# Kernel optimization log

Measured on AMD Instinct MI355X. Metric: run time of the kernel, lower is better.

Reference implementation:

```python
import jax, jax.numpy as jnp
import numpy as np

N_NODES = 50000
N_EDGES = 800000
D = 64
N_GRAPHS = 500  # 100 nodes per graph


def setup_inputs() -> dict:
    key = jax.random.key(0)
    k1, k2, k3, k4, k5, k6 = jax.random.split(key, 6)
    x = jax.random.normal(k1, (N_NODES, D), dtype=jnp.float32)
    edge_index = jax.random.randint(k2, (2, N_EDGES), 0, N_NODES, dtype=jnp.int32)
    split_n = jnp.full((N_GRAPHS,), N_NODES // N_GRAPHS, dtype=jnp.int32)
    # edge_att_mlp: Linear(2*D, 1)
    W_edge = jax.random.normal(k3, (2 * D, 1), dtype=jnp.float32) * 0.05
    b_edge = jax.random.normal(k4, (1,), dtype=jnp.float32) * 0.05
    # node_att_cov: GCNConv(D, 1)
    W_gcn = jax.random.normal(k5, (D, 1), dtype=jnp.float32) * 0.05
    b_gcn = jax.random.normal(k6, (1,), dtype=jnp.float32) * 0.05
    return {"x": x, "edge_index": edge_index, "split_n": split_n,
            "W_edge": W_edge, "b_edge": b_edge, "W_gcn": W_gcn, "b_gcn": b_gcn}


def _segment_softmax(v, seg, num_segments):
    # softmax over dim 0 within each segment (replaces lazy_soft's python loop)
    m = jax.ops.segment_max(v, seg, num_segments=num_segments)
    e = jnp.exp(v - m[seg])
    s = jax.ops.segment_sum(e, seg, num_segments=num_segments)
    return e / s[seg]


def reference(x, edge_index, split_n, W_edge, b_edge, W_gcn, b_gcn):
    n = x.shape[0]
    row, col = edge_index[0], edge_index[1]

    # edge attention: gather pair, linear, sigmoid
    edge_rep = jnp.concatenate([x[row], x[col]], axis=-1)  # [E, 2D]
    edge_att = jax.nn.sigmoid(edge_rep @ W_edge + b_edge)  # [E, 1]
    edge_att_m = edge_att
    edge_att_s = 1.0 - edge_att

    # GCNConv(D, 1): add self-loops, symmetric deg^-1/2 norm, linear, scatter-sum
    h = x @ W_gcn  # [N, 1]
    loop = jnp.arange(n, dtype=row.dtype)
    src = jnp.concatenate([row, loop])
    dst = jnp.concatenate([col, loop])
    deg = jnp.zeros((n,), dtype=x.dtype).at[dst].add(1.0)
    dinv = jax.lax.rsqrt(deg)  # deg >= 1 due to self-loops
    norm = dinv[src] * dinv[dst]  # [E+N]
    node_att = jax.ops.segment_sum(norm[:, None] * h[src], dst, num_segments=n) + b_gcn

    # per-graph ragged softmax (fused segment softmax)
    seg = jnp.repeat(jnp.arange(split_n.shape[0]), split_n, total_repeat_length=n)
    node_att_m = _segment_softmax(node_att, seg, split_n.shape[0])
    node_att_s = _segment_softmax(1.0 - node_att_m, seg, split_n.shape[0])
    return edge_att_m, edge_att_s, node_att_m, node_att_s
```

## Files before the change

### kernel.cpp

```cpp
#include <hip/hip_runtime.h>
#include <math.h>


#define RANGE_S 16384
#define RANGE_H 32768
#define BD_H 1024
#define SOFT_LDS_CAP 2048

typedef unsigned short u16t;
typedef unsigned int u32t;

__global__ __launch_bounds__(BD_H)
void k1_node_hist(const float* __restrict__ x,
                  const float* __restrict__ W_edge,
                  const float* __restrict__ W_gcn,
                  const int* __restrict__ ei,
                  float* __restrict__ pa, float* __restrict__ pb,
                  float* __restrict__ hbuf,
                  u16t* __restrict__ pd,
                  int N, int E, int Ch, int Rh, int CHh, int nodeBlocks, int vec) {
    __shared__ u32t t32[RANGE_H / 2];
    const int bid = blockIdx.x, tid = threadIdx.x;
    if (bid < nodeBlocks) {
        float4* Wsh = (float4*)t32;
        if (tid < 32) Wsh[tid] = ((const float4*)W_edge)[tid];
        else if (tid < 48) Wsh[tid] = ((const float4*)W_gcn)[tid - 32];
        __syncthreads();
        int lane = tid & 15;
        long long gid = (long long)bid * BD_H + tid;
        int i = (int)(gid >> 4);
        if (i >= N) return;
        float4 v = ((const float4*)(x + (size_t)i * 64))[lane];
        float4 wa = Wsh[lane], wb = Wsh[16 + lane], wg = Wsh[32 + lane];
        float p1 = v.x*wa.x + v.y*wa.y + v.z*wa.z + v.w*wa.w;
        float p2 = v.x*wb.x + v.y*wb.y + v.z*wb.z + v.w*wb.w;
        float p3 = v.x*wg.x + v.y*wg.y + v.z*wg.z + v.w*wg.w;
#pragma unroll
        for (int s = 1; s < 16; s <<= 1) {
            p1 += __shfl_xor(p1, s);
            p2 += __shfl_xor(p2, s);
            p3 += __shfl_xor(p3, s);
        }
        if (lane == 0) {
            pa[i] = p1;
            pb[i] = p2;
            hbuf[i] = p3;
        }
        return;
    }
    const int hb = bid - nodeBlocks;
    const int c = hb / Rh;
    const int r = hb - c * Rh;
    const int lo = r * RANGE_H;
    for (int j = tid; j < RANGE_H / 2; j += BD_H) t32[j] = 0u;
    __syncthreads();
    const int e_lo = c * CHh;
    const int e_hi = (E < e_lo + CHh) ? E : (e_lo + CHh);
    const int* __restrict__ col = ei + E;
    for (int e = e_lo + tid * 4; e < e_hi; e += BD_H * 4) {
        if (vec && e + 3 < e_hi) {
            int4 cc = *(const int4*)(col + e);
            unsigned u;
            u = (unsigned)(cc.x - lo); if (u < RANGE_H) atomicAdd(&t32[u >> 1], 1u << ((u & 1) << 4));
            u = (unsigned)(cc.y - lo); if (u < RANGE_H) atomicAdd(&t32[u >> 1], 1u << ((u & 1) << 4));
            u = (unsigned)(cc.z - lo); if (u < RANGE_H) atomicAdd(&t32[u >> 1], 1u << ((u & 1) << 4));
            u = (unsigned)(cc.w - lo); if (u < RANGE_H) atomicAdd(&t32[u >> 1], 1u << ((u & 1) << 4));
        } else {
            int ee = (e_hi < e + 4) ? e_hi : e + 4;
            for (int q = e; q < ee; ++q) {
                unsigned u = (unsigned)(col[q] - lo);
                if (u < RANGE_H) atomicAdd(&t32[u >> 1], 1u << ((u & 1) << 4));
            }
        }
    }
    __syncthreads();
    const size_t base = (size_t)c * N;
    for (int j = tid; j < RANGE_H; j += BD_H) {
        int node = lo + j;
        if (node < N)
            pd[base + node] = (u16t)(t32[j >> 1] >> ((j & 1) << 4));
    }
}

__global__ __launch_bounds__(256)
void k2_dinv_sig(const int* __restrict__ ei,
                 const float* __restrict__ pa, const float* __restrict__ pb,
                 const float* __restrict__ b_edge,
                 const u16t* __restrict__ pd,
                 float* __restrict__ hbuf,
                 float* __restrict__ dv1,
                 float* __restrict__ om, float* __restrict__ os,
                 int N, int E, int Ch, int dinvBlocks, int vec) {
    const int bid = blockIdx.x, tid = threadIdx.x;
    if (bid < dinvBlocks) {
        int i = bid * 256 + tid;
        if (i >= N) return;
        unsigned d0 = 1u, d1 = 0u, d2 = 0u, d3 = 0u;
        int c = 0;
        for (; c + 3 < Ch; c += 4) {
            d0 += pd[(size_t)(c + 0) * N + i];
            d1 += pd[(size_t)(c + 1) * N + i];
            d2 += pd[(size_t)(c + 2) * N + i];
            d3 += pd[(size_t)(c + 3) * N + i];
        }
        for (; c < Ch; ++c) d0 += pd[(size_t)c * N + i];
        float dv = rsqrtf((float)((d0 + d1) + (d2 + d3)));
        hbuf[i] *= dv;
        dv1[i] = dv;
        return;
    }
    int t = (bid - dinvBlocks) * 256 + tid;
    int e0 = t * 4;
    const float b = b_edge[0];
    if (vec && e0 + 3 < E) {
        int4 r = *(const int4*)(ei + e0);
        int4 c = *(const int4*)(ei + E + e0);
        float4 m;
        m.x = 1.f / (1.f + expf(-(pa[r.x] + pb[c.x] + b)));
        m.y = 1.f / (1.f + expf(-(pa[r.y] + pb[c.y] + b)));
        m.z = 1.f / (1.f + expf(-(pa[r.z] + pb[c.z] + b)));
        m.w = 1.f / (1.f + expf(-(pa[r.w] + pb[c.w] + b)));
        *(float4*)(om + e0) = m;
        *(float4*)(os + e0) = make_float4(1.f - m.x, 1.f - m.y, 1.f - m.z, 1.f - m.w);
    } else if (e0 < E) {
        int ee = (E < e0 + 4) ? E : e0 + 4;
        for (int e = e0; e < ee; ++e) {
            float a = 1.f / (1.f + expf(-(pa[ei[e]] + pb[ei[E + e]] + b)));
            om[e] = a; os[e] = 1.f - a;
        }
    }
}

__global__ __launch_bounds__(BD_H)
void k3_scat(const int* __restrict__ ei,
             const float* __restrict__ g1,
             float* __restrict__ partial,
             int N, int E, int Cs, int Rs, int CHs, int vec) {
    __shared__ float table[RANGE_S];
    const int tid = threadIdx.x;
    const int c = blockIdx.x / Rs;
    const int r = blockIdx.x - c * Rs;
    const int lo = r * RANGE_S;
    for (int j = tid; j < RANGE_S; j += BD_H) table[j] = 0.f;
    __syncthreads();
    const int e_lo = c * CHs;
    const int e_hi = (E < e_lo + CHs) ? E : (e_lo + CHs);
    const int* __restrict__ row = ei;
    const int* __restrict__ col = ei + E;
    for (int e = e_lo + tid * 4; e < e_hi; e += BD_H * 4) {
        if (vec && e + 3 < e_hi) {
            int4 cc = *(const int4*)(col + e);
            int4 rr = *(const int4*)(row + e);
            unsigned u;
            u = (unsigned)(cc.x - lo); if (u < RANGE_S) atomicAdd(&table[u], g1[rr.x]);
            u = (unsigned)(cc.y - lo); if (u < RANGE_S) atomicAdd(&table[u], g1[rr.y]);
            u = (unsigned)(cc.z - lo); if (u < RANGE_S) atomicAdd(&table[u], g1[rr.z]);
            u = (unsigned)(cc.w - lo); if (u < RANGE_S) atomicAdd(&table[u], g1[rr.w]);
        } else {
            int ee = (e_hi < e + 4) ? e_hi : e + 4;
            for (int q = e; q < ee; ++q) {
                unsigned u = (unsigned)(col[q] - lo);
                if (u < RANGE_S) atomicAdd(&table[u], g1[row[q]]);
            }
        }
    }
    __syncthreads();
    const size_t base = (size_t)c * N;
    for (int j = tid; j < RANGE_S; j += BD_H) {
        int node = lo + j;
        if (node < N) partial[base + node] = table[j];
    }
}

__global__ __launch_bounds__(128)
void k4_softmax(const float* __restrict__ hbuf,
                const float* __restrict__ dv1,
                const float* __restrict__ partial,
                float* __restrict__ accfb,
                const int* __restrict__ split_n,
                float* __restrict__ out_m, float* __restrict__ out_s,
                int N, int Cs) {
    __shared__ float red[128];
    __shared__ int ired[128];
    __shared__ int sh_off;
    __shared__ float sv[SOFT_LDS_CAP];
    const int g = blockIdx.x;
    const int tid = threadIdx.x;
    const int BD = blockDim.x;

    int part = 0;
    for (int j = tid; j < g; j += BD) part += split_n[j];
    ired[tid] = part; __syncthreads();
    for (int s = 64; s > 0; s >>= 1) {
        if (tid < s) ired[tid] += ired[tid + s];
        __syncthreads();
    }
    if (tid == 0) sh_off = ired[0];
    __syncthreads();
    const int off = sh_off;
    const int cnt = split_n[g];
    const bool fits = (cnt <= SOFT_LDS_CAP);

    for (int j = tid; j < cnt; j += BD) {
        int node = off + j;
        float s0 = hbuf[node], s1 = 0.f, s2 = 0.f, s3 = 0.f;
        int c = 0;
        for (; c + 3 < Cs; c += 4) {
            s0 += partial[(size_t)(c + 0) * N + node];
            s1 += partial[(size_t)(c + 1) * N + node];
            s2 += partial[(size_t)(c + 2) * N + node];
            s3 += partial[(size_t)(c + 3) * N + node];
        }
        for (; c < Cs; ++c) s0 += partial[(size_t)c * N + node];
        float a = dv1[node] * ((s0 + s1) + (s2 + s3));
        if (fits) sv[j] = a; else accfb[node] = a;
    }
    __syncthreads();

    float mx = -INFINITY;
    for (int j = tid; j < cnt; j += BD) mx = fmaxf(mx, fits ? sv[j] : accfb[off + j]);
    red[tid] = mx; __syncthreads();
    for (int s = 64; s > 0; s >>= 1) {
        if (tid < s) red[tid] = fmaxf(red[tid], red[tid + s]);
        __syncthreads();
    }
    mx = red[0]; __syncthreads();
    float sum = 0.f;
    for (int j = tid; j < cnt; j += BD) sum += expf((fits ? sv[j] : accfb[off + j]) - mx);
    red[tid] = sum; __syncthreads();
    for (int s = 64; s > 0; s >>= 1) {
        if (tid < s) red[tid] += red[tid + s];
        __syncthreads();
    }
    const float inv1 = 1.0f / red[0]; __syncthreads();
    for (int j = tid; j < cnt; j += BD) {
        float mv = expf((fits ? sv[j] : accfb[off + j]) - mx) * inv1;
        out_m[off + j] = mv;
        if (fits) sv[j] = mv;
    }
    __syncthreads();

    float mx2 = -INFINITY;
    for (int j = tid; j < cnt; j += BD)
        mx2 = fmaxf(mx2, 1.0f - (fits ? sv[j] : out_m[off + j]));
    red[tid] = mx2; __syncthreads();
    for (int s = 64; s > 0; s >>= 1) {
        if (tid < s) red[tid] = fmaxf(red[tid], red[tid + s]);
        __syncthreads();
    }
    mx2 = red[0]; __syncthreads();
    float sum2 = 0.f;
    for (int j = tid; j < cnt; j += BD)
        sum2 += expf(1.0f - (fits ? sv[j] : out_m[off + j]) - mx2);
    red[tid] = sum2; __syncthreads();
    for (int s = 64; s > 0; s >>= 1) {
        if (tid < s) red[tid] += red[tid + s];
        __syncthreads();
    }
    const float inv2 = 1.0f / red[0]; __syncthreads();
    for (int j = tid; j < cnt; j += BD)
        out_s[off + j] = expf(1.0f - (fits ? sv[j] : out_m[off + j]) - mx2) * inv2;
}

extern "C" void kernel_launch(void* const* d_in, const int* in_sizes, int n_in,
                              void* d_out, int out_size, void* d_ws, size_t ws_size,
                              hipStream_t stream) {
    const float* x      = (const float*)d_in[0];
    const int*   ei     = (const int*)d_in[1];
    const int*   splitn = (const int*)d_in[2];
    const float* W_edge = (const float*)d_in[3];
    const float* b_edge = (const float*)d_in[4];
    const float* W_gcn  = (const float*)d_in[5];

    const int N = in_sizes[0] / 64;
    const int E = in_sizes[1] / 2;
    const int G = in_sizes[2];

    float* out = (float*)d_out;
    float* edge_m = out;
    float* edge_s = out + E;
    float* node_m = out + 2LL * E;
    float* node_s = out + 2LL * E + N;

    int Cs = 64;
    while (Cs > 2 && (size_t)(5 + Cs) * N * sizeof(float) > ws_size) Cs >>= 1;
    int Ch = 32;
    while ((E + Ch - 1) / Ch >= 65536) Ch <<= 1;
    const int Rs = (N + RANGE_S - 1) / RANGE_S;
    const int Rh = (N + RANGE_H - 1) / RANGE_H;
    const int CHs = (((E + Cs - 1) / Cs) + 3) & ~3;
    const int CHh = (((E + Ch - 1) / Ch) + 3) & ~3;
    const int vec = ((E & 3) == 0) ? 1 : 0;

    float* pa      = (float*)d_ws;
    float* pb      = pa + N;
    float* hbuf    = pb + N;
    float* dv1     = hbuf + N;
    float* accfb   = dv1 + N;
    float* partial = accfb + N;
    u16t*  pd      = (u16t*)partial;

    const int nodeBlocks = (int)(((long long)N * 16 + BD_H - 1) / BD_H);
    const int dinvBlocks = (N + 255) / 256;
    const int sigBlocks  = ((E + 3) / 4 + 255) / 256;

    k1_node_hist<<<nodeBlocks + Rh * Ch, BD_H, 0, stream>>>(
        x, W_edge, W_gcn, ei, pa, pb, hbuf, pd, N, E, Ch, Rh, CHh, nodeBlocks, vec);
    k2_dinv_sig<<<dinvBlocks + sigBlocks, 256, 0, stream>>>(
        ei, pa, pb, b_edge, pd, hbuf, dv1, edge_m, edge_s, N, E, Ch, dinvBlocks, vec);
    k3_scat<<<Rs * Cs, BD_H, 0, stream>>>(ei, hbuf, partial, N, E, Cs, Rs, CHs, vec);
    k4_softmax<<<G, 128, 0, stream>>>(hbuf, dv1, partial, accfb, splitn,
                                      node_m, node_s, N, Cs);
}
```

Baseline: 52.39 us.

## Move edge sigmoid into scatter kernel and reorder histogram blocks first

The edge-attention sigmoid work now launches as extra blocks of the scatter kernel instead of sharing a launch with the degree/dinv pass. The dinv computation becomes its own small kernel. Histogram blocks are placed before node projection blocks in the first kernel so the long atomic work starts earliest, and the histogram edge-chunk count doubles. The aim is to overlap the bandwidth-bound sigmoid pass with the LDS-atomic scatter and balance block scheduling. The cost is a dinv launch that runs alone, more partial-degree rows for dinv to read, and sigmoid blocks competing for CUs with the scatter.

```diff
diff --git a/kernel.cpp b/kernel.cpp
--- a/kernel.cpp
+++ b/kernel.cpp
@@ -11,23 +11,23 @@
 typedef unsigned int u32t;
 
 __global__ __launch_bounds__(BD_H)
-void k1_node_hist(const float* __restrict__ x,
+void k1_hist_node(const float* __restrict__ x,
                   const float* __restrict__ W_edge,
                   const float* __restrict__ W_gcn,
                   const int* __restrict__ ei,
                   float* __restrict__ pa, float* __restrict__ pb,
                   float* __restrict__ hbuf,
                   u16t* __restrict__ pd,
-                  int N, int E, int Ch, int Rh, int CHh, int nodeBlocks, int vec) {
+                  int N, int E, int Ch, int Rh, int CHh, int histBlocks, int vec) {
     __shared__ u32t t32[RANGE_H / 2];
     const int bid = blockIdx.x, tid = threadIdx.x;
-    if (bid < nodeBlocks) {
+    if (bid >= histBlocks) {
         float4* Wsh = (float4*)t32;
         if (tid < 32) Wsh[tid] = ((const float4*)W_edge)[tid];
         else if (tid < 48) Wsh[tid] = ((const float4*)W_gcn)[tid - 32];
         __syncthreads();
         int lane = tid & 15;
-        long long gid = (long long)bid * BD_H + tid;
+        long long gid = (long long)(bid - histBlocks) * BD_H + tid;
         int i = (int)(gid >> 4);
         if (i >= N) return;
         float4 v = ((const float4*)(x + (size_t)i * 64))[lane];
@@ -48,9 +48,8 @@
         }
         return;
     }
-    const int hb = bid - nodeBlocks;
-    const int c = hb / Rh;
-    const int r = hb - c * Rh;
+    const int c = bid / Rh;
+    const int r = bid - c * Rh;
     const int lo = r * RANGE_H;
     for (int j = tid; j < RANGE_H / 2; j += BD_H) t32[j] = 0u;
     __syncthreads();
@@ -83,63 +82,61 @@
 }
 
 __global__ __launch_bounds__(256)
-void k2_dinv_sig(const int* __restrict__ ei,
+void k2_dinv(const u16t* __restrict__ pd,
+             float* __restrict__ hbuf,
+             float* __restrict__ dv1,
+             int N, int Ch) {
+    int i = blockIdx.x * 256 + threadIdx.x;
+    if (i >= N) return;
+    unsigned d0 = 1u, d1 = 0u, d2 = 0u, d3 = 0u;
+    int c = 0;
+    for (; c + 3 < Ch; c += 4) {
+        d0 += pd[(size_t)(c + 0) * N + i];
+        d1 += pd[(size_t)(c + 1) * N + i];
+        d2 += pd[(size_t)(c + 2) * N + i];
+        d3 += pd[(size_t)(c + 3) * N + i];
+    }
+    for (; c < Ch; ++c) d0 += pd[(size_t)c * N + i];
+    float dv = rsqrtf((float)((d0 + d1) + (d2 + d3)));
+    hbuf[i] *= dv;
+    dv1[i] = dv;
+}
+
+__global__ __launch_bounds__(BD_H)
+void k3_scat_sig(const int* __restrict__ ei,
+                 const float* __restrict__ g1,
                  const float* __restrict__ pa, const float* __restrict__ pb,
                  const float* __restrict__ b_edge,
-                 const u16t* __restrict__ pd,
-                 float* __restrict__ hbuf,
-                 float* __restrict__ dv1,
+                 float* __restrict__ partial,
                  float* __restrict__ om, float* __restrict__ os,
-                 int N, int E, int Ch, int dinvBlocks, int vec) {
+                 int N, int E, int Cs, int Rs, int CHs, int scatBlocks, int vec) {
     const int bid = blockIdx.x, tid = threadIdx.x;
-    if (bid < dinvBlocks) {
-        int i = bid * 256 + tid;
-        if (i >= N) return;
-        unsigned d0 = 1u, d1 = 0u, d2 = 0u, d3 = 0u;
-        int c = 0;
-        for (; c + 3 < Ch; c += 4) {
-            d0 += pd[(size_t)(c + 0) * N + i];
-            d1 += pd[(size_t)(c + 1) * N + i];
-            d2 += pd[(size_t)(c + 2) * N + i];
-            d3 += pd[(size_t)(c + 3) * N + i];
-        }
-        for (; c < Ch; ++c) d0 += pd[(size_t)c * N + i];
-        float dv = rsqrtf((float)((d0 + d1) + (d2 + d3)));
-        hbuf[i] *= dv;
-        dv1[i] = dv;
+    if (bid >= scatBlocks) {
+        int t = (bid - scatBlocks) * BD_H + tid;
+        int e0 = t * 4;
+        const float b = b_edge[0];
+        if (vec && e0 + 3 < E) {
+            int4 r = *(const int4*)(ei + e0);
+            int4 c = *(const int4*)(ei + E + e0);
+            float4 m;
+            m.x = 1.f / (1.f + expf(-(pa[r.x] + pb[c.x] + b)));
+            m.y = 1.f / (1.f + expf(-(pa[r.y] + pb[c.y] + b)));
+            m.z = 1.f / (1.f + expf(-(pa[r.z] + pb[c.z] + b)));
+            m.w = 1.f / (1.f + expf(-(pa[r.w] + pb[c.w] + b)));
+            *(float4*)(om + e0) = m;
+            *(float4*)(os + e0) = make_float4(1.f - m.x, 1.f - m.y, 1.f - m.z, 1.f - m.w);
+        } else if (e0 < E) {
+            int ee = (E < e0 + 4) ? E : e0 + 4;
+            for (int e = e0; e < ee; ++e) {
+                float a = 1.f / (1.f + expf(-(pa[ei[e]] + pb[ei[E + e]] + b)));
+                om[e] = a; os[e] = 1.f - a;
+            }
+        }
         return;
     }
-    int t = (bid - dinvBlocks) * 256 + tid;
-    int e0 = t * 4;
-    const float b = b_edge[0];
-    if (vec && e0 + 3 < E) {
-        int4 r = *(const int4*)(ei + e0);
-        int4 c = *(const int4*)(ei + E + e0);
-        float4 m;
-        m.x = 1.f / (1.f + expf(-(pa[r.x] + pb[c.x] + b)));
-        m.y = 1.f / (1.f + expf(-(pa[r.y] + pb[c.y] + b)));
-        m.z = 1.f / (1.f + expf(-(pa[r.z] + pb[c.z] + b)));
-        m.w = 1.f / (1.f + expf(-(pa[r.w] + pb[c.w] + b)));
-        *(float4*)(om + e0) = m;
-        *(float4*)(os + e0) = make_float4(1.f - m.x, 1.f - m.y, 1.f - m.z, 1.f - m.w);
-    } else if (e0 < E) {
-        int ee = (E < e0 + 4) ? E : e0 + 4;
-        for (int e = e0; e < ee; ++e) {
-            float a = 1.f / (1.f + expf(-(pa[ei[e]] + pb[ei[E + e]] + b)));
-            om[e] = a; os[e] = 1.f - a;
-        }
-    }
-}
-
-__global__ __launch_bounds__(BD_H)
-void k3_scat(const int* __restrict__ ei,
-             const float* __restrict__ g1,
-             float* __restrict__ partial,
-             int N, int E, int Cs, int Rs, int CHs, int vec) {
     __shared__ float table[RANGE_S];
-    const int tid = threadIdx.x;
-    const int c = blockIdx.x / Rs;
-    const int r = blockIdx.x - c * Rs;
+    const int c = bid / Rs;
+    const int r = bid - c * Rs;
     const int lo = r * RANGE_S;
     for (int j = tid; j < RANGE_S; j += BD_H) table[j] = 0.f;
     __syncthreads();
@@ -284,7 +281,7 @@
 
     int Cs = 64;
     while (Cs > 2 && (size_t)(5 + Cs) * N * sizeof(float) > ws_size) Cs >>= 1;
-    int Ch = 32;
+    int Ch = 64;
     while ((E + Ch - 1) / Ch >= 65536) Ch <<= 1;
     const int Rs = (N + RANGE_S - 1) / RANGE_S;
     const int Rh = (N + RANGE_H - 1) / RANGE_H;
@@ -300,15 +297,18 @@
     float* partial = accfb + N;
     u16t*  pd      = (u16t*)partial;
 
-    const int nodeBlocks = (int)(((long long)N * 16 + BD_H - 1) / BD_H);
+    const int histBlocks = Rh * Ch;
+    const int projBlocks = (int)(((long long)N * 16 + BD_H - 1) / BD_H);
+    const int scatBlocks = Rs * Cs;
+    const int sigBlocks  = (int)(((long long)E / 4 + BD_H - 1) / BD_H) + ((E & 3) ? 1 : 0);
     const int dinvBlocks = (N + 255) / 256;
-    const int sigBlocks  = ((E + 3) / 4 + 255) / 256;
-
-    k1_node_hist<<<nodeBlocks + Rh * Ch, BD_H, 0, stream>>>(
-        x, W_edge, W_gcn, ei, pa, pb, hbuf, pd, N, E, Ch, Rh, CHh, nodeBlocks, vec);
-    k2_dinv_sig<<<dinvBlocks + sigBlocks, 256, 0, stream>>>(
-        ei, pa, pb, b_edge, pd, hbuf, dv1, edge_m, edge_s, N, E, Ch, dinvBlocks, vec);
-    k3_scat<<<Rs * Cs, BD_H, 0, stream>>>(ei, hbuf, partial, N, E, Cs, Rs, CHs, vec);
+
+    k1_hist_node<<<histBlocks + projBlocks, BD_H, 0, stream>>>(
+        x, W_edge, W_gcn, ei, pa, pb, hbuf, pd, N, E, Ch, Rh, CHh, histBlocks, vec);
+    k2_dinv<<<dinvBlocks, 256, 0, stream>>>(pd, hbuf, dv1, N, Ch);
+    k3_scat_sig<<<scatBlocks + sigBlocks, BD_H, 0, stream>>>(
+        ei, hbuf, pa, pb, b_edge, partial, edge_m, edge_s,
+        N, E, Cs, Rs, CHs, scatBlocks, vec);
     k4_softmax<<<G, 128, 0, stream>>>(hbuf, dv1, partial, accfb, splitn,
                                       node_m, node_s, N, Cs);
 }
```

Measured after the change: 49.84 us. -4.9%, faster.
